# Optimization experiments

Measured on AMD Instinct MI355X. Metric: run time of the kernel, lower is better.

## Reference

```python
import jax, jax.numpy as jnp
import numpy as np

NUM_HEADS = 8
EPS = 1e-5


def setup_inputs() -> dict:
    key = jax.random.key(0)
    ks = jax.random.split(key, 6)
    B, C, H, W = 8, 256, 32, 32
    s = 1.0 / np.sqrt(C)  # fan-in scale for 1x1 conv weights
    return {
        "x": jax.random.normal(ks[0], (B, C, H, W), jnp.float32),
        "Wq": jax.random.normal(ks[1], (C, C), jnp.float32) * s,
        "bq": jnp.zeros((C,), jnp.float32),
        "Wk": jax.random.normal(ks[2], (C, C), jnp.float32) * s,
        "bk": jnp.zeros((C,), jnp.float32),
        "Wv": jax.random.normal(ks[3], (C, C), jnp.float32) * s,
        "bv": jnp.zeros((C,), jnp.float32),
        "Wp": jax.random.normal(ks[4], (C, C), jnp.float32) * s,
        "bp": jnp.zeros((C,), jnp.float32),
        "gamma": jnp.ones((C,), jnp.float32),
        "beta": jnp.zeros((C,), jnp.float32),
    }


def _conv1x1(x, W, b):
    # 1x1 Conv2d == channel-mixing matmul: [B,C,H,W] -> [B,C,H,W]
    return jnp.einsum('oi,bihw->bohw', W, x) + b[None, :, None, None]


def reference(x, Wq, bq, Wk, bk, Wv, bv, Wp, bp, gamma, beta):
    B, C, H, W = x.shape
    nh = NUM_HEADS
    hd = C // nh
    HW = H * W

    q = _conv1x1(x, Wq, bq).reshape(B, nh, hd, HW)
    k = _conv1x1(x, Wk, bk).reshape(B, nh, hd, HW)
    v = _conv1x1(x, Wv, bv).reshape(B, nh, hd, HW)

    scores = jnp.einsum('bhdi,bhdj->bhij', q, k) / (hd ** 0.5)  # [B,nh,HW,HW]
    attn = jax.nn.softmax(scores, axis=-1)
    out = jnp.einsum('bhij,bhdj->bhdi', attn, v).reshape(B, C, H, W)

    out = _conv1x1(out, Wp, bp) + x  # residual

    # LayerNorm over channel dim (channels-last, as in original)
    o = out.transpose(0, 2, 3, 1)  # [B,H,W,C]
    mu = jnp.mean(o, axis=-1, keepdims=True)
    var = jnp.var(o, axis=-1, keepdims=True)
    o = (o - mu) * jax.lax.rsqrt(var + EPS) * gamma + beta
    return o.transpose(0, 3, 1, 2)
```

## Files before the change

### kernel.cpp

```cpp
#include <hip/hip_runtime.h>
#include <math.h>

#define NB 8
#define NC 256
#define NHW 1024
#define NHEADS 8
#define HD 32

typedef _Float16 half_t;
typedef __attribute__((ext_vector_type(8))) _Float16 half8;
typedef __attribute__((ext_vector_type(4))) _Float16 half4v;
typedef __attribute__((ext_vector_type(2))) _Float16 half2v;
typedef __attribute__((ext_vector_type(4))) float floatx4;

__device__ __forceinline__ half2v pk2(float a, float b) {
    union {
        __fp16 __attribute__((ext_vector_type(2))) r;
        half2v h;
    } u;
    u.r = __builtin_amdgcn_cvt_pkrtz(a, b);
    return u.h;
}
__device__ __forceinline__ void st8h(half_t* p, half2v a, half2v b) {
    union { half2v h[2]; uint2 u; } t;
    t.h[0] = a; t.h[1] = b;
    *(uint2*)p = t.u;
}

__global__ __launch_bounds__(256) void prepx(
    const float* __restrict__ Wq, const float* __restrict__ Wk,
    const float* __restrict__ Wv, const float* __restrict__ Wp,
    const float* __restrict__ x, half_t* __restrict__ Wh, half_t* __restrict__ xT)
{
    __shared__ half_t tile[64][66];
    int l = blockIdx.x;
    if (l < 256) {
        int m = l >> 6;
        const float* src = (m == 0) ? Wq : (m == 1) ? Wk : (m == 2) ? Wv : Wp;
        int off = ((l & 63) * 256 + threadIdx.x) * 4;
        float4 v = *(const float4*)&src[off];
        st8h(Wh + (size_t)m * NC * NC + off, pk2(v.x, v.y), pk2(v.z, v.w));
        return;
    }
    l -= 256;
    int t = threadIdx.x;
    int b = l >> 6;
    int i0 = ((l >> 4) & 3) * 64, s0 = (l & 15) * 64;
    const float* xb = x + ((size_t)b * NC + i0) * NHW + s0;
    int s4 = t & 15, il = t >> 4;
    #pragma unroll
    for (int r = 0; r < 4; r++) {
        int i = il + 16 * r;
        float4 v = *(const float4*)&xb[i * NHW + s4 * 4];
        *(half2v*)&tile[i][s4 * 4]     = pk2(v.x, v.y);
        *(half2v*)&tile[i][s4 * 4 + 2] = pk2(v.z, v.w);
    }
    __syncthreads();
    int iv = t & 7, sl = t >> 3;
    half_t* ob = xT + ((size_t)b * NHW + s0) * NC + i0 + iv * 8;
    #pragma unroll
    for (int r = 0; r < 2; r++) {
        int s = sl + 32 * r;
        union { half_t h[8]; int4 v4; } pkd;
        #pragma unroll
        for (int u = 0; u < 8; u++) pkd.h[u] = tile[iv * 8 + u][s];
        *(int4*)&ob[(size_t)s * NC] = pkd.v4;
    }
}

__global__ __launch_bounds__(256) void qkv_mfma(
    const half_t* __restrict__ xT, const half_t* __restrict__ Wh,
    const float* __restrict__ bq, const float* __restrict__ bk, const float* __restrict__ bv,
    half_t* __restrict__ Qt, half_t* __restrict__ Kt, half_t* __restrict__ Vv)
{
    int bz = blockIdx.z;
    int b = bz & 7, p = bz >> 3;
    const half_t* W    = Wh + (size_t)p * NC * NC;
    const float*  bias = (p == 0) ? bq : (p == 1) ? bk : bv;

    int wv = threadIdx.x >> 6, lane = threadIdx.x & 63;
    int mm = lane & 15, q = lane >> 4;
    int o0 = blockIdx.y * 128 + wv * 32;
    int s0 = blockIdx.x * 64;

    const half_t* xb = xT + (size_t)b * NHW * NC;
    floatx4 acc[2][4];
    #pragma unroll
    for (int mt = 0; mt < 2; mt++)
        #pragma unroll
        for (int nt = 0; nt < 4; nt++) acc[mt][nt] = (floatx4){0.f, 0.f, 0.f, 0.f};

    #pragma unroll
    for (int k0 = 0; k0 < NC; k0 += 32) {
        half8 af[2], bf[4];
        #pragma unroll
        for (int mt = 0; mt < 2; mt++)
            af[mt] = *(const half8*)&W[(size_t)(o0 + mt * 16 + mm) * NC + k0 + q * 8];
        #pragma unroll
        for (int nt = 0; nt < 4; nt++)
            bf[nt] = *(const half8*)&xb[(size_t)(s0 + nt * 16 + mm) * NC + k0 + q * 8];
        #pragma unroll
        for (int mt = 0; mt < 2; mt++)
            #pragma unroll
            for (int nt = 0; nt < 4; nt++)
                acc[mt][nt] = __builtin_amdgcn_mfma_f32_16x16x32_f16(af[mt], bf[nt], acc[mt][nt], 0, 0, 0);
    }

    int h  = (o0 >> 5);
    int bh = b * NHEADS + h;
    const float qs = 0.17677669529663687f * 1.4426950408889634f;

    #pragma unroll
    for (int mt = 0; mt < 2; mt++) {
        int d0 = mt * 16 + q * 4;
        float bb[4];
        #pragma unroll
        for (int r = 0; r < 4; r++) bb[r] = bias[o0 + mt * 16 + q * 4 + r];
        #pragma unroll
        for (int nt = 0; nt < 4; nt++) {
            int s = s0 + nt * 16 + mm;
            float v0 = acc[mt][nt][0] + bb[0], v1 = acc[mt][nt][1] + bb[1];
            float v2 = acc[mt][nt][2] + bb[2], v3 = acc[mt][nt][3] + bb[3];
            if (p == 0) { v0 *= qs; v1 *= qs; v2 *= qs; v3 *= qs; }
            if (p < 2) {
                half_t* out = (p == 0 ? Qt : Kt) + ((size_t)bh * NHW + s) * HD + d0;
                st8h(out, pk2(v0, v1), pk2(v2, v3));
            } else {
                Vv[((size_t)bh * HD + d0 + 0) * NHW + s] = (half_t)v0;
                Vv[((size_t)bh * HD + d0 + 1) * NHW + s] = (half_t)v1;
                Vv[((size_t)bh * HD + d0 + 2) * NHW + s] = (half_t)v2;
                Vv[((size_t)bh * HD + d0 + 3) * NHW + s] = (half_t)v3;
            }
        }
    }
}

__global__ __launch_bounds__(256) void attn_mfma(
    const half_t* __restrict__ Qt, const half_t* __restrict__ Kt,
    const half_t* __restrict__ Vv, half_t* __restrict__ At)
{
    __shared__ half_t Pl[4][2][2][16][36];
    __shared__ float Oz[4][32][34];
    __shared__ float Dz[4][32];

    int wv = threadIdx.x >> 6, lane = threadIdx.x & 63;
    int mm = lane & 15, q = lane >> 4;
    int L = blockIdx.x;
    int bh = L & 63, iblk = L >> 6;
    int b = bh >> 3, h = bh & 7;
    int i0 = iblk * 32;

    const half_t* Qb = Qt + (size_t)bh * NHW * HD;
    const half_t* Kb = Kt + (size_t)bh * NHW * HD;
    const half_t* Vb = Vv + (size_t)bh * HD * NHW;

    half8 qf0 = *(const half8*)&Qb[(size_t)(i0 + mm) * HD + q * 8];
    half8 qf1 = *(const half8*)&Qb[(size_t)(i0 + 16 + mm) * HD + q * 8];

    const int jb = wv * 256;
    floatx4 zero = (floatx4){0.f, 0.f, 0.f, 0.f};
    floatx4 oa00 = zero, oa01 = zero, oa10 = zero, oa11 = zero;
    float d0 = 0.f, d1 = 0.f;
    const _Float16 z = (_Float16)0.f;
    half8 pf_p0 = {z, z, z, z, z, z, z, z}, pf_p1 = pf_p0;

    half8 kc0 = *(const half8*)&Kb[(size_t)(jb + mm) * HD + q * 8];
    half8 kc1 = *(const half8*)&Kb[(size_t)(jb + 16 + mm) * HD + q * 8];
    half8 kn0 = *(const half8*)&Kb[(size_t)(jb + 32 + mm) * HD + q * 8];
    half8 kn1 = *(const half8*)&Kb[(size_t)(jb + 48 + mm) * HD + q * 8];
    half8 vc0 = *(const half8*)&Vb[(size_t)mm * NHW + jb + q * 8];
    half8 vc1 = *(const half8*)&Vb[(size_t)(16 + mm) * NHW + jb + q * 8];
    half8 vp0 = vc0, vp1 = vc1;

    #pragma unroll
    for (int it = 0; it < 8; it++) {
        floatx4 s00 = __builtin_amdgcn_mfma_f32_16x16x32_f16(kc0, qf0, zero, 0, 0, 0);
        floatx4 s01 = __builtin_amdgcn_mfma_f32_16x16x32_f16(kc1, qf0, zero, 0, 0, 0);
        floatx4 s10 = __builtin_amdgcn_mfma_f32_16x16x32_f16(kc0, qf1, zero, 0, 0, 0);
        floatx4 s11 = __builtin_amdgcn_mfma_f32_16x16x32_f16(kc1, qf1, zero, 0, 0, 0);

        int jk = jb + ((it + 2) & 7) * 32;
        int jv = jb + ((it + 1) & 7) * 32;
        half8 kf0 = *(const half8*)&Kb[(size_t)(jk + mm) * HD + q * 8];
        half8 kf1 = *(const half8*)&Kb[(size_t)(jk + 16 + mm) * HD + q * 8];
        half8 vn0 = *(const half8*)&Vb[(size_t)mm * NHW + jv + q * 8];
        half8 vn1 = *(const half8*)&Vb[(size_t)(16 + mm) * NHW + jv + q * 8];

        oa00 = __builtin_amdgcn_mfma_f32_16x16x32_f16(vp0, pf_p0, oa00, 0, 0, 0);
        oa01 = __builtin_amdgcn_mfma_f32_16x16x32_f16(vp1, pf_p0, oa01, 0, 0, 0);
        oa10 = __builtin_amdgcn_mfma_f32_16x16x32_f16(vp0, pf_p1, oa10, 0, 0, 0);
        oa11 = __builtin_amdgcn_mfma_f32_16x16x32_f16(vp1, pf_p1, oa11, 0, 0, 0);

        int buf = it & 1;
        {
            float e0 = exp2f(s00[0]), e1 = exp2f(s00[1]);
            float e2 = exp2f(s00[2]), e3 = exp2f(s00[3]);
            float f0 = exp2f(s01[0]), f1 = exp2f(s01[1]);
            float f2 = exp2f(s01[2]), f3 = exp2f(s01[3]);
            d0 += ((e0 + e1) + (e2 + e3)) + ((f0 + f1) + (f2 + f3));
            half_t (*PB)[36] = Pl[wv][0][buf];
            st8h(&PB[mm][q * 4],      pk2(e0, e1), pk2(e2, e3));
            st8h(&PB[mm][16 + q * 4], pk2(f0, f1), pk2(f2, f3));
        }
        {
            float e0 = exp2f(s10[0]), e1 = exp2f(s10[1]);
            float e2 = exp2f(s10[2]), e3 = exp2f(s10[3]);
            float f0 = exp2f(s11[0]), f1 = exp2f(s11[1]);
            float f2 = exp2f(s11[2]), f3 = exp2f(s11[3]);
            d1 += ((e0 + e1) + (e2 + e3)) + ((f0 + f1) + (f2 + f3));
            half_t (*PB)[36] = Pl[wv][1][buf];
            st8h(&PB[mm][q * 4],      pk2(e0, e1), pk2(e2, e3));
            st8h(&PB[mm][16 + q * 4], pk2(f0, f1), pk2(f2, f3));
        }
        union { half4v h4[2]; half8 h8; } u0, u1;
        u0.h4[0] = *(half4v*)&Pl[wv][0][buf][mm][q * 8];
        u0.h4[1] = *(half4v*)&Pl[wv][0][buf][mm][q * 8 + 4];
        u1.h4[0] = *(half4v*)&Pl[wv][1][buf][mm][q * 8];
        u1.h4[1] = *(half4v*)&Pl[wv][1][buf][mm][q * 8 + 4];

        kc0 = kn0; kc1 = kn1; kn0 = kf0; kn1 = kf1;
        vp0 = vc0; vp1 = vc1; vc0 = vn0; vc1 = vn1;
        pf_p0 = u0.h8; pf_p1 = u1.h8;
    }
    oa00 = __builtin_amdgcn_mfma_f32_16x16x32_f16(vp0, pf_p0, oa00, 0, 0, 0);
    oa01 = __builtin_amdgcn_mfma_f32_16x16x32_f16(vp1, pf_p0, oa01, 0, 0, 0);
    oa10 = __builtin_amdgcn_mfma_f32_16x16x32_f16(vp0, pf_p1, oa10, 0, 0, 0);
    oa11 = __builtin_amdgcn_mfma_f32_16x16x32_f16(vp1, pf_p1, oa11, 0, 0, 0);

    d0 += __shfl_xor(d0, 16); d0 += __shfl_xor(d0, 32);
    d1 += __shfl_xor(d1, 16); d1 += __shfl_xor(d1, 32);

    #pragma unroll
    for (int r = 0; r < 4; r++) {
        Oz[wv][q * 4 + r][mm]           = oa00[r];
        Oz[wv][16 + q * 4 + r][mm]      = oa01[r];
        Oz[wv][q * 4 + r][16 + mm]      = oa10[r];
        Oz[wv][16 + q * 4 + r][16 + mm] = oa11[r];
    }
    if (q == 0) { Dz[wv][mm] = d0; Dz[wv][16 + mm] = d1; }
    __syncthreads();

    int t = threadIdx.x;
    int iloc = t >> 3, dg = t & 7;
    float den = (Dz[0][iloc] + Dz[1][iloc]) + (Dz[2][iloc] + Dz[3][iloc]);
    float rinv = 1.f / den;
    float v[4];
    #pragma unroll
    for (int r = 0; r < 4; r++) {
        int d = dg * 4 + r;
        v[r] = ((Oz[0][d][iloc] + Oz[1][d][iloc]) + (Oz[2][d][iloc] + Oz[3][d][iloc])) * rinv;
    }
    half_t* dst = At + ((size_t)b * NHW + i0 + iloc) * NC + h * HD + dg * 4;
    st8h(dst, pk2(v[0], v[1]), pk2(v[2], v[3]));
}

__global__ __launch_bounds__(512) void projln(
    const half_t* __restrict__ At, const half_t* __restrict__ Wh,
    const float* __restrict__ bp, const float* __restrict__ x,
    const float* __restrict__ gamma, const float* __restrict__ beta,
    float* __restrict__ outp)
{
    __shared__ float tile[16][273];
    __shared__ float xs[256][17];
    __shared__ float Pz[4][64][17];
    __shared__ float ps[32][16], ps2[32][16];
    __shared__ float mu_s[16], rs_s[16];

    int t = threadIdx.x, wv = t >> 6, lane = t & 63;
    int mm = lane & 15, q = lane >> 4;
    int oh = wv & 3, kh = wv >> 2;
    int o0 = oh * 64;
    int b = blockIdx.y, s0 = blockIdx.x * 16;
    const half_t* ab  = At + (size_t)b * NHW * NC;
    const half_t* Wpp = Wh + (size_t)3 * NC * NC;

    {
        int sL = t & 15, cb = t >> 4;
        #pragma unroll
        for (int pass = 0; pass < 8; pass++) {
            int c = pass * 32 + cb;
            xs[c][sL] = x[((size_t)b * NC + c) * NHW + s0 + sL];
        }
    }

    floatx4 acc[4];
    #pragma unroll
    for (int mt = 0; mt < 4; mt++) acc[mt] = (floatx4){0.f, 0.f, 0.f, 0.f};

    int kbase = kh * 128;
    #pragma unroll
    for (int kk = 0; kk < 128; kk += 32) {
        int k0 = kbase + kk;
        half8 bf = *(const half8*)&ab[(size_t)(s0 + mm) * NC + k0 + q * 8];
        #pragma unroll
        for (int mt = 0; mt < 4; mt++) {
            half8 af = *(const half8*)&Wpp[(size_t)(o0 + mt * 16 + mm) * NC + k0 + q * 8];
            acc[mt] = __builtin_amdgcn_mfma_f32_16x16x32_f16(af, bf, acc[mt], 0, 0, 0);
        }
    }

    if (kh == 1) {
        #pragma unroll
        for (int mt = 0; mt < 4; mt++)
            #pragma unroll
            for (int r = 0; r < 4; r++)
                Pz[oh][mt * 16 + q * 4 + r][mm] = acc[mt][r];
    }
    __syncthreads();
    if (kh == 0) {
        #pragma unroll
        for (int mt = 0; mt < 4; mt++) {
            #pragma unroll
            for (int r = 0; r < 4; r++) {
                int ol = mt * 16 + q * 4 + r;
                int o = o0 + ol;
                tile[mm][o] = acc[mt][r] + Pz[oh][ol][mm] + bp[o] + xs[o][mm];
            }
        }
    }
    __syncthreads();

    int sL = t & 15, part = t >> 4;
    float sum = 0.f, sq = 0.f;
    #pragma unroll
    for (int cc = 0; cc < 8; cc++) {
        float v = tile[sL][part * 8 + cc];
        sum += v; sq += v * v;
    }
    ps[part][sL] = sum; ps2[part][sL] = sq;
    __syncthreads();
    if (t < 16) {
        float S = 0.f, S2 = 0.f;
        #pragma unroll
        for (int p2 = 0; p2 < 32; p2++) { S += ps[p2][t]; S2 += ps2[p2][t]; }
        float mu  = S * (1.f / NC);
        float var = S2 * (1.f / NC) - mu * mu;
        mu_s[t] = mu;
        rs_s[t] = rsqrtf(var + 1e-5f);
    }
    __syncthreads();
    float mu = mu_s[sL], rs = rs_s[sL];
    float* ob = outp + (size_t)b * NC * NHW;
    #pragma unroll
    for (int cc = 0; cc < 8; cc++) {
        int c = part * 8 + cc;
        ob[(size_t)c * NHW + s0 + sL] = (tile[sL][c] - mu) * rs * gamma[c] + beta[c];
    }
}

extern "C" void kernel_launch(void* const* d_in, const int* in_sizes, int n_in,
                              void* d_out, int out_size, void* d_ws, size_t ws_size,
                              hipStream_t stream)
{
    const float* x     = (const float*)d_in[0];
    const float* Wq    = (const float*)d_in[1];
    const float* bq    = (const float*)d_in[2];
    const float* Wk    = (const float*)d_in[3];
    const float* bk    = (const float*)d_in[4];
    const float* Wv    = (const float*)d_in[5];
    const float* bv    = (const float*)d_in[6];
    const float* Wp    = (const float*)d_in[7];
    const float* bp    = (const float*)d_in[8];
    const float* gamma = (const float*)d_in[9];
    const float* beta  = (const float*)d_in[10];
    float* out = (float*)d_out;

    char* w = (char*)d_ws;
    half_t* xT = (half_t*)(w);
    half_t* Qt = (half_t*)(w + ((size_t)4  << 20));
    half_t* Kt = (half_t*)(w + ((size_t)8  << 20));
    half_t* Vv = (half_t*)(w + ((size_t)12 << 20));
    half_t* At = (half_t*)(w + ((size_t)16 << 20));
    half_t* Wh = (half_t*)(w + ((size_t)20 << 20));

    prepx<<<dim3(768), 256, 0, stream>>>(Wq, Wk, Wv, Wp, x, Wh, xT);
    qkv_mfma<<<dim3(16, 2, 24), 256, 0, stream>>>(xT, Wh, bq, bk, bv, Qt, Kt, Vv);
    attn_mfma<<<dim3(2048), 256, 0, stream>>>(Qt, Kt, Vv, At);
    projln<<<dim3(64, 8), 512, 0, stream>>>(At, Wh, bp, x, gamma, beta, out);
}
```

Before: 141.6 us.

## Fuse x transpose/convert and weight fp16 conversion into GEMM kernels

Removes the separate prepx kernel. qkv_mfma now loads fp32 x directly, converts it to fp16 and transposes it into shared memory, and both GEMM kernels read fp32 weights and convert them in registers. This saves one launch and the write and re-read of the fp16 xT and weight buffers. In exchange, weight conversion is repeated in every block and each weight fetch moves twice as many bytes from global memory, and each qkv block redoes the x staging that prepx did once.

```diff
diff --git a/kernel.cpp b/kernel.cpp
--- a/kernel.cpp
+++ b/kernel.cpp
@@ -26,64 +26,51 @@
     t.h[0] = a; t.h[1] = b;
     *(uint2*)p = t.u;
 }
-
-__global__ __launch_bounds__(256) void prepx(
-    const float* __restrict__ Wq, const float* __restrict__ Wk,
-    const float* __restrict__ Wv, const float* __restrict__ Wp,
-    const float* __restrict__ x, half_t* __restrict__ Wh, half_t* __restrict__ xT)
-{
-    __shared__ half_t tile[64][66];
-    int l = blockIdx.x;
-    if (l < 256) {
-        int m = l >> 6;
-        const float* src = (m == 0) ? Wq : (m == 1) ? Wk : (m == 2) ? Wv : Wp;
-        int off = ((l & 63) * 256 + threadIdx.x) * 4;
-        float4 v = *(const float4*)&src[off];
-        st8h(Wh + (size_t)m * NC * NC + off, pk2(v.x, v.y), pk2(v.z, v.w));
-        return;
-    }
-    l -= 256;
-    int t = threadIdx.x;
-    int b = l >> 6;
-    int i0 = ((l >> 4) & 3) * 64, s0 = (l & 15) * 64;
-    const float* xb = x + ((size_t)b * NC + i0) * NHW + s0;
-    int s4 = t & 15, il = t >> 4;
-    #pragma unroll
-    for (int r = 0; r < 4; r++) {
-        int i = il + 16 * r;
-        float4 v = *(const float4*)&xb[i * NHW + s4 * 4];
-        *(half2v*)&tile[i][s4 * 4]     = pk2(v.x, v.y);
-        *(half2v*)&tile[i][s4 * 4 + 2] = pk2(v.z, v.w);
-    }
-    __syncthreads();
-    int iv = t & 7, sl = t >> 3;
-    half_t* ob = xT + ((size_t)b * NHW + s0) * NC + i0 + iv * 8;
-    #pragma unroll
-    for (int r = 0; r < 2; r++) {
-        int s = sl + 32 * r;
-        union { half_t h[8]; int4 v4; } pkd;
-        #pragma unroll
-        for (int u = 0; u < 8; u++) pkd.h[u] = tile[iv * 8 + u][s];
-        *(int4*)&ob[(size_t)s * NC] = pkd.v4;
-    }
+__device__ __forceinline__ half8 ldw8(const float* p) {
+    float4 w0 = *(const float4*)p;
+    float4 w1 = *(const float4*)(p + 4);
+    union { half2v h2[4]; half8 h8; } u;
+    u.h2[0] = pk2(w0.x, w0.y); u.h2[1] = pk2(w0.z, w0.w);
+    u.h2[2] = pk2(w1.x, w1.y); u.h2[3] = pk2(w1.z, w1.w);
+    return u.h8;
 }
 
 __global__ __launch_bounds__(256) void qkv_mfma(
-    const half_t* __restrict__ xT, const half_t* __restrict__ Wh,
+    const float* __restrict__ x,
+    const float* __restrict__ Wq, const float* __restrict__ Wk, const float* __restrict__ Wv,
     const float* __restrict__ bq, const float* __restrict__ bk, const float* __restrict__ bv,
     half_t* __restrict__ Qt, half_t* __restrict__ Kt, half_t* __restrict__ Vv)
 {
+    __shared__ half_t xs[64][264];
+
     int bz = blockIdx.z;
     int b = bz & 7, p = bz >> 3;
-    const half_t* W    = Wh + (size_t)p * NC * NC;
-    const float*  bias = (p == 0) ? bq : (p == 1) ? bk : bv;
-
-    int wv = threadIdx.x >> 6, lane = threadIdx.x & 63;
+    const float* W    = (p == 0) ? Wq : (p == 1) ? Wk : Wv;
+    const float* bias = (p == 0) ? bq : (p == 1) ? bk : bv;
+
+    int t = threadIdx.x;
+    int s0 = blockIdx.x * 64;
+    const float* xb = x + (size_t)b * NC * NHW;
+
+    {
+        int sf = t & 15, cp = t >> 4;
+        #pragma unroll
+        for (int pass = 0; pass < 8; pass++) {
+            int c = cp * 2 + 32 * pass;
+            float4 a  = *(const float4*)&xb[(size_t)c * NHW + s0 + sf * 4];
+            float4 bb = *(const float4*)&xb[(size_t)(c + 1) * NHW + s0 + sf * 4];
+            *(half2v*)&xs[sf * 4 + 0][c] = pk2(a.x, bb.x);
+            *(half2v*)&xs[sf * 4 + 1][c] = pk2(a.y, bb.y);
+            *(half2v*)&xs[sf * 4 + 2][c] = pk2(a.z, bb.z);
+            *(half2v*)&xs[sf * 4 + 3][c] = pk2(a.w, bb.w);
+        }
+    }
+    __syncthreads();
+
+    int wv = t >> 6, lane = t & 63;
     int mm = lane & 15, q = lane >> 4;
     int o0 = blockIdx.y * 128 + wv * 32;
-    int s0 = blockIdx.x * 64;
-
-    const half_t* xb = xT + (size_t)b * NHW * NC;
+
     floatx4 acc[2][4];
     #pragma unroll
     for (int mt = 0; mt < 2; mt++)
@@ -95,10 +82,10 @@
         half8 af[2], bf[4];
         #pragma unroll
         for (int mt = 0; mt < 2; mt++)
-            af[mt] = *(const half8*)&W[(size_t)(o0 + mt * 16 + mm) * NC + k0 + q * 8];
+            af[mt] = ldw8(&W[(size_t)(o0 + mt * 16 + mm) * NC + k0 + q * 8]);
         #pragma unroll
         for (int nt = 0; nt < 4; nt++)
-            bf[nt] = *(const half8*)&xb[(size_t)(s0 + nt * 16 + mm) * NC + k0 + q * 8];
+            bf[nt] = *(const half8*)&xs[nt * 16 + mm][k0 + q * 8];
         #pragma unroll
         for (int mt = 0; mt < 2; mt++)
             #pragma unroll
@@ -255,7 +242,7 @@
 }
 
 __global__ __launch_bounds__(512) void projln(
-    const half_t* __restrict__ At, const half_t* __restrict__ Wh,
+    const half_t* __restrict__ At, const float* __restrict__ Wp,
     const float* __restrict__ bp, const float* __restrict__ x,
     const float* __restrict__ gamma, const float* __restrict__ beta,
     float* __restrict__ outp)
@@ -271,8 +258,7 @@
     int oh = wv & 3, kh = wv >> 2;
     int o0 = oh * 64;
     int b = blockIdx.y, s0 = blockIdx.x * 16;
-    const half_t* ab  = At + (size_t)b * NHW * NC;
-    const half_t* Wpp = Wh + (size_t)3 * NC * NC;
+    const half_t* ab = At + (size_t)b * NHW * NC;
 
     {
         int sL = t & 15, cb = t >> 4;
@@ -294,7 +280,7 @@
         half8 bf = *(const half8*)&ab[(size_t)(s0 + mm) * NC + k0 + q * 8];
         #pragma unroll
         for (int mt = 0; mt < 4; mt++) {
-            half8 af = *(const half8*)&Wpp[(size_t)(o0 + mt * 16 + mm) * NC + k0 + q * 8];
+            half8 af = ldw8(&Wp[(size_t)(o0 + mt * 16 + mm) * NC + k0 + q * 8]);
             acc[mt] = __builtin_amdgcn_mfma_f32_16x16x32_f16(af, bf, acc[mt], 0, 0, 0);
         }
     }
@@ -366,15 +352,12 @@
     float* out = (float*)d_out;
 
     char* w = (char*)d_ws;
-    half_t* xT = (half_t*)(w);
-    half_t* Qt = (half_t*)(w + ((size_t)4  << 20));
-    half_t* Kt = (half_t*)(w + ((size_t)8  << 20));
-    half_t* Vv = (half_t*)(w + ((size_t)12 << 20));
-    half_t* At = (half_t*)(w + ((size_t)16 << 20));
-    half_t* Wh = (half_t*)(w + ((size_t)20 << 20));
-
-    prepx<<<dim3(768), 256, 0, stream>>>(Wq, Wk, Wv, Wp, x, Wh, xT);
-    qkv_mfma<<<dim3(16, 2, 24), 256, 0, stream>>>(xT, Wh, bq, bk, bv, Qt, Kt, Vv);
+    half_t* Qt = (half_t*)(w);
+    half_t* Kt = (half_t*)(w + ((size_t)4  << 20));
+    half_t* Vv = (half_t*)(w + ((size_t)8  << 20));
+    half_t* At = (half_t*)(w + ((size_t)12 << 20));
+
+    qkv_mfma<<<dim3(16, 2, 24), 256, 0, stream>>>(x, Wq, Wk, Wv, bq, bk, bv, Qt, Kt, Vv);
     attn_mfma<<<dim3(2048), 256, 0, stream>>>(Qt, Kt, Vv, At);
-    projln<<<dim3(64, 8), 512, 0, stream>>>(At, Wh, bp, x, gamma, beta, out);
-}
+    projln<<<dim3(64, 8), 512, 0, stream>>>(At, Wp, bp, x, gamma, beta, out);
+}
```

After: 140.1 us. No clear change (-1.0%).
